# Kernel tuning notes

Hardware: AMD Instinct MI355X
Metric: run time of the kernel (lower is better)

Reference implementation:

```python
import jax, jax.numpy as jnp
import numpy as np

B, S, H, A = 64, 200, 256, 16
CAPS_LAYERS = 3
NEG = -1e9
LN_EPS = 1e-12


def _layernorm(x, g, b):
    mu = jnp.mean(x, axis=-1, keepdims=True)
    var = jnp.mean(jnp.square(x - mu), axis=-1, keepdims=True)
    return (x - mu) / jnp.sqrt(var + LN_EPS) * g + b


def setup_inputs() -> dict:
    key = jax.random.key(0)
    ks = jax.random.split(key, 10)
    s = 0.02  # initializer_range
    return {
        "item_emb": jax.random.normal(ks[0], (B, S, H), jnp.float32),
        "item_seq": jax.random.randint(ks[1], (B, S), 0, 50000),
        "time_seq": jax.random.randint(ks[2], (B, S, 2), 0, 14),
        "W_lin": s * jax.random.normal(ks[3], (H, H), jnp.float32),
        "b_lin": jnp.zeros((H,), jnp.float32),
        "aspect_embs": s * jax.random.normal(ks[4], (A, H), jnp.float32),
        "pos_emb": s * jax.random.normal(ks[5], (S, H), jnp.float32),
        "tdt_emb": s * jax.random.normal(ks[6], (14, H), jnp.float32),
        "tdn_emb": s * jax.random.normal(ks[7], (14, H), jnp.float32),
        "Wa1": s * jax.random.normal(ks[8], (H, H), jnp.float32),
        "ba1": jnp.zeros((H,), jnp.float32),
        "Wa2": s * jax.random.normal(ks[9], (H,), jnp.float32),
        "ba2": jnp.zeros((1,), jnp.float32),
        "ln_g": jnp.ones((H,), jnp.float32),
        "ln_b": jnp.zeros((H,), jnp.float32),
    }


def reference(item_emb, item_seq, time_seq, W_lin, b_lin, aspect_embs,
              pos_emb, tdt_emb, tdn_emb, Wa1, ba1, Wa2, ba2, ln_g, ln_b):
    b, s = item_emb.shape[0], item_emb.shape[1]
    pad = item_seq == 0  # [B,S]

    # ---- TimeAwareAttention (seq_output has a singleton neighbor dim in torch) ----
    td = tdt_emb[time_seq[:, :, 0]] + tdn_emb[time_seq[:, :, 1]]       # [B,S,H]
    tma_in = pos_emb[None, :s] + item_emb + td                          # [B,S,H]
    h = tma_in @ Wa1 + ba1
    h = jnp.where(h >= 0, h, 0.01 * h)                                  # LeakyReLU
    w = h @ Wa2 + ba2[0]                                                # [B,S]
    w = jnp.where(pad, NEG, w)
    tma = jax.nn.softmax(w, axis=-1)                                    # [B,S]

    # ---- gating (eval: clean gates) ----
    gates = jnp.einsum('bsh,ah->bsa', item_emb, aspect_embs)            # [B,S,A]
    idx = jnp.argmax(gates, axis=-1)                                    # topk k=1, [B,S]

    src = jnp.where(pad, 0.0, 1.0)
    counts = jnp.zeros((b, A), jnp.float32).at[jnp.arange(b)[:, None], idx].add(src)
    aspect_mask = counts == 0                                           # [B,A]

    # ---- item transform (dropout = identity in eval) ----
    moe = _layernorm(jnp.tanh(item_emb @ W_lin + b_lin) + item_emb, ln_g, ln_b)  # [B,S,H]

    # ---- capsule routing ----
    bij = gates
    cap = jnp.broadcast_to(aspect_embs[None], (b, A, H))
    for _ in range(CAPS_LAYERS):
        cij = jnp.where(aspect_mask[:, None, :], NEG, bij)
        cij = jax.nn.softmax(cij, axis=-1)
        cij = jnp.where(pad[:, :, None], 0.0, cij)                      # [B,S,A]
        cap = jnp.einsum('bsa,bsh,bs->bah', cij, moe, tma)              # [B,A,H]
        n2 = jnp.sum(jnp.square(cap), axis=-1, keepdims=True)
        cap = n2 / (1.0 + n2) / jnp.sqrt(n2 + 1e-9) * cap               # squash
        bij = bij + jnp.einsum('bsh,bah->bsa', moe, cap)

    # ---- gather activated interests / activation positions ----
    activated = cap[jnp.arange(b)[:, None], idx]                        # [B,S,H]
    seq_pos = jnp.where(pad, 0, jnp.arange(1, s + 1)[None, :]).astype(jnp.float32)
    act_mat = jnp.full((b, s, A), -1.0, jnp.float32)
    act_mat = act_mat.at[jnp.arange(b)[:, None], jnp.arange(s)[None, :], idx].set(seq_pos)
    act_mat = jnp.where(pad[:, :, None], -1.0, act_mat)
    max_pos = jnp.max(act_mat, axis=1)                                  # [B,A]
    aspects_item_idx = jnp.where(max_pos > -1.0, max_pos - 1.0, max_pos)

    gates_sm = jax.nn.softmax(gates, axis=-1)
    return (cap, gates_sm, aspect_mask, activated, aspects_item_idx, idx[:, :, None])
```

## Files before the change

### kernel.cpp

```cpp
#include <hip/hip_runtime.h>

#define B_ 64
#define S_ 200
#define H_ 256
#define A_ 16
#define M_ (B_*S_)
#define NEGV (-1000000000.0f)

typedef unsigned short ushortT;
typedef __attribute__((ext_vector_type(8))) short short8;
typedef __attribute__((ext_vector_type(4))) float f32x4;

__device__ __forceinline__ ushortT bf16u(float f) {
  unsigned int u = __builtin_bit_cast(unsigned int, f);
  unsigned int r = (u + 0x7fffu + ((u >> 16) & 1u)) >> 16;
  return (ushortT)r;
}
__device__ __forceinline__ float bf2f(ushortT u) {
  unsigned int v = ((unsigned int)u) << 16;
  return __builtin_bit_cast(float, v);
}

__global__ __launch_bounds__(256) void prepT_kernel(
    const float* __restrict__ Wa1, const float* __restrict__ W_lin,
    ushortT* __restrict__ Wa1T, ushortT* __restrict__ WlinT)
{
  __shared__ float T[64*65];
  const int blk = blockIdx.x, t = threadIdx.x;
  int wsel = blk >> 4;
  int tile = blk & 15;
  const float* W = wsel ? W_lin : Wa1;
  ushortT* WT = wsel ? WlinT : Wa1T;
  int tr = (tile >> 2) * 64, tc = (tile & 3) * 64;
  #pragma unroll
  for (int p = 0; p < 16; ++p) {
    int r = p*4 + (t >> 6);
    int c = t & 63;
    T[c*65 + r] = W[(tr + r)*H_ + tc + c];
  }
  __syncthreads();
  #pragma unroll
  for (int p = 0; p < 16; ++p) {
    int n = p*4 + (t >> 6);
    int k = t & 63;
    WT[(tc + n)*H_ + tr + k] = bf16u(T[n*65 + k]);
  }
}

__global__ __launch_bounds__(512) void fused_kernel(
    const float* __restrict__ item, const int* __restrict__ iseq,
    const int* __restrict__ tseq, const float* __restrict__ pos,
    const float* __restrict__ tdt, const float* __restrict__ tdn,
    const float* __restrict__ asp,
    const ushortT* __restrict__ Wa1T, const ushortT* __restrict__ WlinT,
    const float* __restrict__ ba1, const float* __restrict__ Wa2,
    const float* __restrict__ ba2, const float* __restrict__ b_lin,
    const float* __restrict__ g_ln, const float* __restrict__ b_ln,
    float* __restrict__ w_out, ushortT* __restrict__ moe_outB,
    float* __restrict__ graw, float* __restrict__ gates_sm,
    float* __restrict__ idxf)
{
  __shared__ __align__(16) ushortT smem[51200];
  __shared__ int sL[64], ttL[64], tnL[64];
  __shared__ float wp[2][64], ln1[2][64], ln2[2][64], mus[64], rss[64];

  const int t = threadIdx.x;
  const int m0 = blockIdx.x * 64;
  const int lane = t & 63, w = t >> 6;
  const int g = w >> 2, wl = w & 3;
  const int wm = wl >> 1, wn = wl & 1;
  const int col = lane & 15;
  const int rg  = lane >> 4;

  if (t < 64) {
    int m = m0 + t;
    sL[t]  = m % S_;
    ttL[t] = tseq[2*m];
    tnL[t] = tseq[2*m+1];
  }
  __syncthreads();

  const int arow = t >> 3;
  const int ac4  = (t & 7) * 4;
  const int nr   = t >> 1;
  const int kh   = (t & 1) * 16;
  const int srow = sL[arow], trow = ttL[arow], nrow = tnL[arow];

  ushortT* const Atma0 = smem;
  ushortT* const Aitm0 = smem + 5120;
  ushortT* const B0b   = smem + 10240;
  ushortT* const B1b   = smem + 30720;

  float4 pi = *(const float4*)&item[(size_t)(m0+arow)*H_ + ac4];
  float4 pp = *(const float4*)&pos[srow*H_ + ac4];
  float4 pt = *(const float4*)&tdt[trow*H_ + ac4];
  float4 pn = *(const float4*)&tdn[nrow*H_ + ac4];
  uint4 b0a = *(const uint4*)&Wa1T[(size_t)nr*H_ + kh];
  uint4 b0b = *(const uint4*)&Wa1T[(size_t)nr*H_ + kh + 8];
  uint4 b1a = *(const uint4*)&WlinT[(size_t)nr*H_ + kh];
  uint4 b1b = *(const uint4*)&WlinT[(size_t)nr*H_ + kh + 8];
  {
    union { ushortT u[4]; uint2 v; } ci, ct;
    ci.u[0] = bf16u(pi.x); ci.u[1] = bf16u(pi.y);
    ci.u[2] = bf16u(pi.z); ci.u[3] = bf16u(pi.w);
    ct.u[0] = bf16u(pi.x + pp.x + pt.x + pn.x);
    ct.u[1] = bf16u(pi.y + pp.y + pt.y + pn.y);
    ct.u[2] = bf16u(pi.z + pp.z + pt.z + pn.z);
    ct.u[3] = bf16u(pi.w + pp.w + pt.w + pn.w);
    *(uint2*)&Aitm0[arow*40 + ac4] = ci.v;
    *(uint2*)&Atma0[arow*40 + ac4] = ct.v;
    *(uint4*)&B0b[nr*40 + kh]     = b0a;
    *(uint4*)&B0b[nr*40 + kh + 8] = b0b;
    *(uint4*)&B1b[nr*40 + kh]     = b1a;
    *(uint4*)&B1b[nr*40 + kh + 8] = b1b;
  }
  __syncthreads();

  f32x4 acc[2][8];
  #pragma unroll
  for (int r = 0; r < 2; ++r)
    #pragma unroll
    for (int q = 0; q < 8; ++q) acc[r][q] = (f32x4){0.f,0.f,0.f,0.f};

  #pragma unroll
  for (int ks = 0; ks < 8; ++ks) {
    if (ks < 7) {
      const int k1 = (ks + 1) * 32;
      pi = *(const float4*)&item[(size_t)(m0+arow)*H_ + k1 + ac4];
      pp = *(const float4*)&pos[srow*H_ + k1 + ac4];
      pt = *(const float4*)&tdt[trow*H_ + k1 + ac4];
      pn = *(const float4*)&tdn[nrow*H_ + k1 + ac4];
      b0a = *(const uint4*)&Wa1T[(size_t)nr*H_ + k1 + kh];
      b0b = *(const uint4*)&Wa1T[(size_t)nr*H_ + k1 + kh + 8];
      b1a = *(const uint4*)&WlinT[(size_t)nr*H_ + k1 + kh];
      b1b = *(const uint4*)&WlinT[(size_t)nr*H_ + k1 + kh + 8];
    }
    {
      const int p = ks & 1;
      const ushortT* Ab = (g ? Aitm0 : Atma0) + p*2560;
      const ushortT* Bb = (g ? B1b : B0b) + p*10240;
      short8 af0 = *(const short8*)&Ab[(wm*32 + col)*40 + rg*8];
      short8 af1 = *(const short8*)&Ab[(wm*32 + 16 + col)*40 + rg*8];
      #pragma unroll
      for (int q = 0; q < 8; ++q) {
        short8 bf = *(const short8*)&Bb[(wn*128 + q*16 + col)*40 + rg*8];
        acc[0][q] = __builtin_amdgcn_mfma_f32_16x16x32_bf16(af0, bf, acc[0][q], 0, 0, 0);
        acc[1][q] = __builtin_amdgcn_mfma_f32_16x16x32_bf16(af1, bf, acc[1][q], 0, 0, 0);
      }
    }
    if (ks < 7) {
      const int p = (ks + 1) & 1;
      union { ushortT u[4]; uint2 v; } ci, ct;
      ci.u[0] = bf16u(pi.x); ci.u[1] = bf16u(pi.y);
      ci.u[2] = bf16u(pi.z); ci.u[3] = bf16u(pi.w);
      ct.u[0] = bf16u(pi.x + pp.x + pt.x + pn.x);
      ct.u[1] = bf16u(pi.y + pp.y + pt.y + pn.y);
      ct.u[2] = bf16u(pi.z + pp.z + pt.z + pn.z);
      ct.u[3] = bf16u(pi.w + pp.w + pt.w + pn.w);
      *(uint2*)&(Aitm0 + p*2560)[arow*40 + ac4] = ci.v;
      *(uint2*)&(Atma0 + p*2560)[arow*40 + ac4] = ct.v;
      ushortT* B0w = B0b + p*10240;
      ushortT* B1w = B1b + p*10240;
      *(uint4*)&B0w[nr*40 + kh]     = b0a;
      *(uint4*)&B0w[nr*40 + kh + 8] = b0b;
      *(uint4*)&B1w[nr*40 + kh]     = b1a;
      *(uint4*)&B1w[nr*40 + kh + 8] = b1b;
    }
    __syncthreads();
  }

  float* aspl = (float*)smem;
  float* gL   = (float*)smem + 4160;
  #pragma unroll
  for (int i = 0; i < 2; ++i) {
    int e = t + 512*i;
    int r = e >> 6, c = e & 63;
    *(float4*)&aspl[r*260 + 4*c] = *(const float4*)&asp[r*H_ + 4*c];
  }

  float glv[8], bbv[8];
  if (g == 0) {
    float bav[8], wav[8];
    #pragma unroll
    for (int q = 0; q < 8; ++q) {
      int n = wn*128 + q*16 + col;
      bav[q] = ba1[n]; wav[q] = Wa2[n];
    }
    #pragma unroll
    for (int r = 0; r < 2; ++r)
      #pragma unroll
      for (int j = 0; j < 4; ++j) {
        float p = 0.f;
        #pragma unroll
        for (int q = 0; q < 8; ++q) {
          float h = acc[r][q][j] + bav[q];
          h = (h >= 0.f) ? h : 0.01f*h;
          p += h * wav[q];
        }
        #pragma unroll
        for (int mk = 1; mk < 16; mk <<= 1) p += __shfl_xor(p, mk);
        if (col == 0) wp[wn][wm*32 + r*16 + rg*4 + j] = p;
      }
  } else {
    float blv[8];
    #pragma unroll
    for (int q = 0; q < 8; ++q) {
      int n = wn*128 + q*16 + col;
      blv[q] = b_lin[n]; glv[q] = g_ln[n]; bbv[q] = b_ln[n];
    }
    #pragma unroll
    for (int r = 0; r < 2; ++r)
      #pragma unroll
      for (int j = 0; j < 4; ++j) {
        int row = wm*32 + r*16 + rg*4 + j;
        float s1 = 0.f, s2 = 0.f;
        #pragma unroll
        for (int q = 0; q < 8; ++q) {
          int n = wn*128 + q*16 + col;
          float vv = tanhf(acc[r][q][j] + blv[q]) + item[(size_t)(m0+row)*H_ + n];
          acc[r][q][j] = vv; s1 += vv; s2 += vv*vv;
        }
        #pragma unroll
        for (int mk = 1; mk < 16; mk <<= 1) {
          s1 += __shfl_xor(s1, mk);
          s2 += __shfl_xor(s2, mk);
        }
        if (col == 0) { ln1[wn][row] = s1; ln2[wn][row] = s2; }
      }
  }
  __syncthreads();
  if (t < 64) {
    int row = t, m = m0 + row;
    w_out[m] = (iseq[m] == 0) ? NEGV : (wp[0][row] + wp[1][row] + ba2[0]);
  } else if (t < 128) {
    int row = t - 64;
    float s1 = ln1[0][row] + ln1[1][row];
    float s2 = ln2[0][row] + ln2[1][row];
    float mu  = s1 * (1.0f/H_);
    float var = s2 * (1.0f/H_) - mu*mu;
    mus[row] = mu;
    rss[row] = 1.0f / sqrtf(fmaxf(var, 0.f) + 1e-12f);
  }
  __syncthreads();
  if (g == 1) {
    #pragma unroll
    for (int r = 0; r < 2; ++r)
      #pragma unroll
      for (int j = 0; j < 4; ++j) {
        int row = wm*32 + r*16 + rg*4 + j;
        int m = m0 + row;
        float mu = mus[row], rs = rss[row];
        #pragma unroll
        for (int q = 0; q < 8; ++q) {
          int n = wn*128 + q*16 + col;
          moe_outB[(size_t)m*H_ + n] = bf16u((acc[r][q][j] - mu)*rs*glv[q] + bbv[q]);
        }
      }
  }

  {
    const int a  = t & 15;
    const int r2 = (t >> 4) * 2;
    float ga = 0.f, gb = 0.f;
    const float* x0p = &item[(size_t)(m0 + r2)*H_];
    const float* x1p = &item[(size_t)(m0 + r2 + 1)*H_];
    #pragma unroll 8
    for (int k4 = 0; k4 < 64; ++k4) {
      float4 av = *(const float4*)&aspl[a*260 + 4*k4];
      float4 x0 = *(const float4*)&x0p[4*k4];
      float4 x1 = *(const float4*)&x1p[4*k4];
      ga += x0.x*av.x + x0.y*av.y + x0.z*av.z + x0.w*av.w;
      gb += x1.x*av.x + x1.y*av.y + x1.z*av.z + x1.w*av.w;
    }
    gL[r2*20 + a]       = ga;
    gL[(r2 + 1)*20 + a] = gb;
  }
  __syncthreads();
  if (t < 64) {
    float row[16];
    #pragma unroll
    for (int a = 0; a < 16; ++a) row[a] = gL[t*20 + a];
    float best = row[0]; int bi = 0;
    #pragma unroll
    for (int a = 1; a < 16; ++a)
      if (row[a] > best) { best = row[a]; bi = a; }
    idxf[m0 + t] = (float)bi;
    float mx = row[0];
    #pragma unroll
    for (int a = 1; a < 16; ++a) mx = fmaxf(mx, row[a]);
    float ex[16], sm = 0.f;
    #pragma unroll
    for (int a = 0; a < 16; ++a) { ex[a] = expf(row[a] - mx); sm += ex[a]; }
    float inv = 1.f / sm;
    #pragma unroll
    for (int q = 0; q < 4; ++q) {
      float4 rv; rv.x = row[4*q]; rv.y = row[4*q+1]; rv.z = row[4*q+2]; rv.w = row[4*q+3];
      *(float4*)&graw[(m0+t)*A_ + 4*q] = rv;
      float4 o; o.x = ex[4*q]*inv; o.y = ex[4*q+1]*inv; o.z = ex[4*q+2]*inv; o.w = ex[4*q+3]*inv;
      *(float4*)&gates_sm[(m0+t)*A_ + 4*q] = o;
    }
  }
}

__device__ __forceinline__ float blk_max(float v, float* red) {
  #pragma unroll
  for (int mk = 32; mk; mk >>= 1) v = fmaxf(v, __shfl_xor(v, mk));
  int t = threadIdx.x;
  if ((t & 63) == 0) red[t >> 6] = v;
  __syncthreads();
  if (t < 64) {
    float x = (t < 16) ? red[t] : -3.0e38f;
    #pragma unroll
    for (int mk = 8; mk; mk >>= 1) x = fmaxf(x, __shfl_xor(x, mk));
    if (t == 0) red[0] = x;
  }
  __syncthreads();
  float r = red[0];
  __syncthreads();
  return r;
}

__device__ __forceinline__ float blk_sum(float v, float* red) {
  #pragma unroll
  for (int mk = 32; mk; mk >>= 1) v += __shfl_xor(v, mk);
  int t = threadIdx.x;
  if ((t & 63) == 0) red[t >> 6] = v;
  __syncthreads();
  if (t < 64) {
    float x = (t < 16) ? red[t] : 0.f;
    #pragma unroll
    for (int mk = 8; mk; mk >>= 1) x += __shfl_xor(x, mk);
    if (t == 0) red[0] = x;
  }
  __syncthreads();
  float r = red[0];
  __syncthreads();
  return r;
}

#define WGSTR 232
#define CBSTR 260
#define CLSTR 252

__global__ __launch_bounds__(1024) void phaseC_kernel(
    const int* __restrict__ iseq, const float* __restrict__ w_in,
    const ushortT* __restrict__ moeB, const float* __restrict__ idxf,
    const float* __restrict__ graw,
    float* __restrict__ cap_out,
    float* __restrict__ mask_out,
    float* __restrict__ aidx_out)
{
  __shared__ ushortT moeTr[57344];
  __shared__ ushortT wgtT[16*WGSTR];
  __shared__ ushortT capB[16*CBSTR];
  __shared__ float bij[4032];
  __shared__ float n2p[16*17];
  __shared__ float n2s[16];
  __shared__ float tmaL[S_];
  __shared__ float red[16];
  __shared__ float maskf[A_];
  __shared__ int counts[A_], maxpos[A_];
  __shared__ int idxl[S_];
  __shared__ int padl[S_];

  const int t = threadIdx.x;
  const int b = blockIdx.x;
  const int base = b * S_;
  const int lane = t & 63, w = t >> 6;
  const int la = lane & 15, lg = lane >> 4;

  #pragma unroll
  for (int u = 0; u < 4; ++u) {
    int e = t + 1024*u;
    if (e < 3584) {
      int ht = e & 15, s = e >> 4;
      int ks = s >> 5, s4l = (s >> 2) & 7, sr = s & 3;
      int bp = (s4l & 1) ? 4 + (s4l >> 1) : (s4l >> 1);
      int li = ((ht*7 + ks)*8 + bp)*64 + sr*16;
      if (s < S_) {
        const ushortT* gp = &moeB[((size_t)(base + s))*H_ + ht*16];
        *(uint4*)&moeTr[li]     = *(const uint4*)gp;
        *(uint4*)&moeTr[li + 8] = *(const uint4*)(gp + 8);
      } else {
        uint4 z = {0,0,0,0};
        *(uint4*)&moeTr[li] = z; *(uint4*)&moeTr[li + 8] = z;
      }
    }
  }
  if (t < 512) {
    int a = t >> 5, s = 200 + (t & 31);
    wgtT[a*WGSTR + s] = 0;
  }

  if (t < A_) { counts[t] = 0; maxpos[t] = -1; }
  float wv = -3.0e38f;
  if (t < S_) {
    int s = t;
    padl[s] = (iseq[base+s] == 0) ? 1 : 0;
    idxl[s] = (int)idxf[base+s];
    wv = w_in[base+s];
    #pragma unroll
    for (int q = 0; q < 4; ++q)
      *(float4*)&bij[s*20 + 4*q] = *(const float4*)&graw[(base+s)*A_ + 4*q];
  }
  __syncthreads();

  short8 a2[7];
  {
    unsigned vA = (unsigned)(w*7168 + lane*8);
    #pragma unroll
    for (int ks = 0; ks < 7; ++ks) {
      long long r0, r1;
      asm volatile(
        "ds_read_b64_tr_b16 %0, %2\n\t"
        "ds_read_b64_tr_b16 %1, %2 offset:512\n\t"
        "s_waitcnt lgkmcnt(0)"
        : "=&v"(r0), "=&v"(r1) : "v"(vA + (unsigned)(ks*1024)) : "memory");
      __builtin_amdgcn_sched_barrier(0);
      union { short8 v; long long q[2]; } uu;
      uu.q[0] = r0; uu.q[1] = r1;
      a2[ks] = uu.v;
    }
  }

  if (t < S_ && !padl[t]) {
    atomicAdd(&counts[idxl[t]], 1);
    atomicMax(&maxpos[idxl[t]], t + 1);
  }
  float mxw = blk_max(wv, red);
  float ev = (t < S_) ? expf(wv - mxw) : 0.f;
  float sw = blk_sum(ev, red);
  if (t < S_) tmaL[t] = ev / sw;
  __syncthreads();
  if (t < A_) {
    int c = counts[t];
    float mkv = (c == 0) ? 1.f : 0.f;
    maskf[t] = mkv;
    mask_out[b*A_ + t] = mkv;
    int mp = maxpos[t];
    aidx_out[b*A_ + t] = (mp > 0) ? (float)(mp - 1) : -1.f;
  }
  __syncthreads();

  for (int iter = 0; iter < 3; ++iter) {
    #pragma unroll
    for (int pass = 0; pass < 4; ++pass) {
      int s = pass*64 + (t >> 4);
      int a = t & 15;
      if (s < S_) {
        float v = bij[s*20 + a];
        v = (maskf[a] > 0.5f) ? NEGV : v;
        float mx = v;
        #pragma unroll
        for (int mk = 1; mk < 16; mk <<= 1) mx = fmaxf(mx, __shfl_xor(mx, mk));
        float e = expf(v - mx);
        float sm = e;
        #pragma unroll
        for (int mk = 1; mk < 16; mk <<= 1) sm += __shfl_xor(sm, mk);
        float sc = (padl[s] ? 0.f : tmaL[s]) / sm;
        wgtT[a*WGSTR + s] = bf16u(e*sc);
      }
    }
    __syncthreads();

    f32x4 acc = (f32x4){0.f,0.f,0.f,0.f};
    #pragma unroll
    for (int ks = 0; ks < 7; ++ks) {
      short8 bf = *(const short8*)&wgtT[la*WGSTR + ks*32 + lg*8];
      acc = __builtin_amdgcn_mfma_f32_16x16x32_bf16(a2[ks], bf, acc, 0, 0, 0);
    }
    {
      float n2 = acc[0]*acc[0] + acc[1]*acc[1] + acc[2]*acc[2] + acc[3]*acc[3];
      n2 += __shfl_xor(n2, 16);
      n2 += __shfl_xor(n2, 32);
      if (lane < 16) n2p[w*17 + lane] = n2;
    }
    __syncthreads();
    if (t < 16) {
      float sv = 0.f;
      #pragma unroll
      for (int w2 = 0; w2 < 16; ++w2) sv += n2p[w2*17 + t];
      n2s[t] = sv / (1.f + sv) / sqrtf(sv + 1e-9f);
    }
    __syncthreads();
    {
      float sc = n2s[la];
      if (iter < 2) {
        #pragma unroll
        for (int r = 0; r < 4; ++r)
          capB[la*CBSTR + w*16 + lg*4 + r] = bf16u(acc[r]*sc);
      } else {
        float* capl = bij;
        #pragma unroll
        for (int r = 0; r < 4; ++r)
          capl[la*CLSTR + w*16 + lg*4 + r] = acc[r]*sc;
      }
    }
    __syncthreads();

    if (iter < 2) {
      if (w < 13) {
        int sR = w*16 + la;
        int ksS = sR >> 5, s4l = (sR >> 2) & 7, sr = sR & 3;
        int bp = (s4l & 1) ? 4 + (s4l >> 1) : (s4l >> 1);
        int laneA = ksS*512 + bp*64 + sr*16 + (lg & 1)*8 + (lg >> 1)*3584;
        f32x4 accS = (f32x4){0.f,0.f,0.f,0.f};
        #pragma unroll
        for (int k4 = 0; k4 < 8; ++k4) {
          short8 am = *(const short8*)&moeTr[laneA + k4*7168];
          short8 bc = *(const short8*)&capB[la*CBSTR + k4*32 + lg*8];
          accS = __builtin_amdgcn_mfma_f32_16x16x32_bf16(am, bc, accS, 0, 0, 0);
        }
        int sW = w*16 + lg*4;
        #pragma unroll
        for (int r = 0; r < 4; ++r)
          if (sW + r < S_) bij[(sW + r)*20 + la] += accS[r];
      }
      __syncthreads();
    }
  }

  {
    const float* capl = bij;
    int a = t >> 6, h4 = t & 63;
    float4 v = *(const float4*)&capl[a*CLSTR + 4*h4];
    *(float4*)&cap_out[((size_t)b*A_ + a)*H_ + 4*h4] = v;
  }
}

__global__ __launch_bounds__(256) void gather_kernel(
    const float* __restrict__ capv, const float* __restrict__ idxf,
    float* __restrict__ act)
{
  int e4 = blockIdx.x * 256 + threadIdx.x;
  int m = e4 >> 6, h4 = e4 & 63;
  int b = m / S_;
  int id = (int)idxf[m];
  float4 v = *(const float4*)&capv[((b*A_) + id)*H_ + 4*h4];
  *(float4*)&act[(size_t)4*e4] = v;
}

extern "C" void kernel_launch(void* const* d_in, const int* in_sizes, int n_in,
                              void* d_out, int out_size, void* d_ws, size_t ws_size,
                              hipStream_t stream) {
  (void)in_sizes; (void)n_in; (void)out_size; (void)ws_size;
  const float* item  = (const float*)d_in[0];
  const int*   iseq  = (const int*)d_in[1];
  const int*   tseq  = (const int*)d_in[2];
  const float* W_lin = (const float*)d_in[3];
  const float* b_lin = (const float*)d_in[4];
  const float* asp   = (const float*)d_in[5];
  const float* pos   = (const float*)d_in[6];
  const float* tdt   = (const float*)d_in[7];
  const float* tdn   = (const float*)d_in[8];
  const float* Wa1   = (const float*)d_in[9];
  const float* ba1   = (const float*)d_in[10];
  const float* Wa2   = (const float*)d_in[11];
  const float* ba2   = (const float*)d_in[12];
  const float* g_ln  = (const float*)d_in[13];
  const float* b_ln  = (const float*)d_in[14];

  float* out    = (float*)d_out;
  float* cap_o  = out;
  float* gate_o = out + 262144;
  float* mask_o = out + 466944;
  float* act_o  = out + 467968;
  float* aidx_o = out + 3744768;
  float* idx_o  = out + 3745792;

  ushortT* moeB  = (ushortT*)d_ws;
  ushortT* Wa1T  = (ushortT*)((char*)d_ws + 6553600);
  ushortT* WlinT = (ushortT*)((char*)d_ws + 6553600 + 131072);
  float*   w_ws  = (float*)((char*)d_ws + 6553600 + 262144);
  float*   graw  = (float*)((char*)d_ws + 6553600 + 262144 + 51200);

  prepT_kernel<<<32, 256, 0, stream>>>(Wa1, W_lin, Wa1T, WlinT);
  fused_kernel<<<200, 512, 0, stream>>>(item, iseq, tseq, pos, tdt, tdn, asp,
      Wa1T, WlinT, ba1, Wa2, ba2, b_lin, g_ln, b_ln, w_ws, moeB,
      graw, gate_o, idx_o);
  phaseC_kernel<<<B_, 1024, 0, stream>>>(iseq, w_ws, moeB, idx_o, graw,
      cap_o, mask_o, aidx_o);
  gather_kernel<<<(M_*H_/4)/256, 256, 0, stream>>>(cap_o, idx_o, act_o);
}
```

Measured before the change: 62.73 us.

## Load GEMM B fragments directly to registers and fuse gather into phaseC

The fused kernel now loads the transposed weight fragments for its MFMAs straight from global memory into double-buffered registers instead of staging them through shared memory. This cuts LDS usage from about 100KB to about 22KB and adds a launch bound requesting two blocks per CU. Separately, the activated-interest gather is folded into the end of phaseC, which reads capsules from shared memory and drops a separate kernel launch. The trade-offs are more global weight traffic per wave (each wave re-reads its fragments) and more register pressure, plus a longer tail in phaseC with only 64 blocks writing the large act output.

New measurement: 66.71 us. 6.3% more time.

```diff
diff --git a/kernel.cpp b/kernel.cpp
--- a/kernel.cpp
+++ b/kernel.cpp
@@ -47,7 +47,7 @@
   }
 }
 
-__global__ __launch_bounds__(512) void fused_kernel(
+__global__ __launch_bounds__(512, 2) void fused_kernel(
     const float* __restrict__ item, const int* __restrict__ iseq,
     const int* __restrict__ tseq, const float* __restrict__ pos,
     const float* __restrict__ tdt, const float* __restrict__ tdn,
@@ -60,7 +60,7 @@
     float* __restrict__ graw, float* __restrict__ gates_sm,
     float* __restrict__ idxf)
 {
-  __shared__ __align__(16) ushortT smem[51200];
+  __shared__ __align__(16) ushortT smem[11264];
   __shared__ int sL[64], ttL[64], tnL[64];
   __shared__ float wp[2][64], ln1[2][64], ln2[2][64], mus[64], rss[64];
 
@@ -82,23 +82,22 @@
 
   const int arow = t >> 3;
   const int ac4  = (t & 7) * 4;
-  const int nr   = t >> 1;
-  const int kh   = (t & 1) * 16;
   const int srow = sL[arow], trow = ttL[arow], nrow = tnL[arow];
 
   ushortT* const Atma0 = smem;
   ushortT* const Aitm0 = smem + 5120;
-  ushortT* const B0b   = smem + 10240;
-  ushortT* const B1b   = smem + 30720;
+
+  const ushortT* __restrict__ WTp = g ? WlinT : Wa1T;
 
   float4 pi = *(const float4*)&item[(size_t)(m0+arow)*H_ + ac4];
   float4 pp = *(const float4*)&pos[srow*H_ + ac4];
   float4 pt = *(const float4*)&tdt[trow*H_ + ac4];
   float4 pn = *(const float4*)&tdn[nrow*H_ + ac4];
-  uint4 b0a = *(const uint4*)&Wa1T[(size_t)nr*H_ + kh];
-  uint4 b0b = *(const uint4*)&Wa1T[(size_t)nr*H_ + kh + 8];
-  uint4 b1a = *(const uint4*)&WlinT[(size_t)nr*H_ + kh];
-  uint4 b1b = *(const uint4*)&WlinT[(size_t)nr*H_ + kh + 8];
+  short8 bfr[2][8];
+  #pragma unroll
+  for (int q = 0; q < 8; ++q)
+    bfr[0][q] = *(const short8*)&WTp[(size_t)(wn*128 + q*16 + col)*H_ + rg*8];
+
   {
     union { ushortT u[4]; uint2 v; } ci, ct;
     ci.u[0] = bf16u(pi.x); ci.u[1] = bf16u(pi.y);
@@ -109,10 +108,6 @@
     ct.u[3] = bf16u(pi.w + pp.w + pt.w + pn.w);
     *(uint2*)&Aitm0[arow*40 + ac4] = ci.v;
     *(uint2*)&Atma0[arow*40 + ac4] = ct.v;
-    *(uint4*)&B0b[nr*40 + kh]     = b0a;
-    *(uint4*)&B0b[nr*40 + kh + 8] = b0b;
-    *(uint4*)&B1b[nr*40 + kh]     = b1a;
-    *(uint4*)&B1b[nr*40 + kh + 8] = b1b;
   }
   __syncthreads();
 
@@ -130,22 +125,19 @@
       pp = *(const float4*)&pos[srow*H_ + k1 + ac4];
       pt = *(const float4*)&tdt[trow*H_ + k1 + ac4];
       pn = *(const float4*)&tdn[nrow*H_ + k1 + ac4];
-      b0a = *(const uint4*)&Wa1T[(size_t)nr*H_ + k1 + kh];
-      b0b = *(const uint4*)&Wa1T[(size_t)nr*H_ + k1 + kh + 8];
-      b1a = *(const uint4*)&WlinT[(size_t)nr*H_ + k1 + kh];
-      b1b = *(const uint4*)&WlinT[(size_t)nr*H_ + k1 + kh + 8];
+      #pragma unroll
+      for (int q = 0; q < 8; ++q)
+        bfr[(ks+1)&1][q] = *(const short8*)&WTp[(size_t)(wn*128 + q*16 + col)*H_ + k1 + rg*8];
     }
     {
       const int p = ks & 1;
       const ushortT* Ab = (g ? Aitm0 : Atma0) + p*2560;
-      const ushortT* Bb = (g ? B1b : B0b) + p*10240;
       short8 af0 = *(const short8*)&Ab[(wm*32 + col)*40 + rg*8];
       short8 af1 = *(const short8*)&Ab[(wm*32 + 16 + col)*40 + rg*8];
       #pragma unroll
       for (int q = 0; q < 8; ++q) {
-        short8 bf = *(const short8*)&Bb[(wn*128 + q*16 + col)*40 + rg*8];
-        acc[0][q] = __builtin_amdgcn_mfma_f32_16x16x32_bf16(af0, bf, acc[0][q], 0, 0, 0);
-        acc[1][q] = __builtin_amdgcn_mfma_f32_16x16x32_bf16(af1, bf, acc[1][q], 0, 0, 0);
+        acc[0][q] = __builtin_amdgcn_mfma_f32_16x16x32_bf16(af0, bfr[ks&1][q], acc[0][q], 0, 0, 0);
+        acc[1][q] = __builtin_amdgcn_mfma_f32_16x16x32_bf16(af1, bfr[ks&1][q], acc[1][q], 0, 0, 0);
       }
     }
     if (ks < 7) {
@@ -159,12 +151,6 @@
       ct.u[3] = bf16u(pi.w + pp.w + pt.w + pn.w);
       *(uint2*)&(Aitm0 + p*2560)[arow*40 + ac4] = ci.v;
       *(uint2*)&(Atma0 + p*2560)[arow*40 + ac4] = ct.v;
-      ushortT* B0w = B0b + p*10240;
-      ushortT* B1w = B1b + p*10240;
-      *(uint4*)&B0w[nr*40 + kh]     = b0a;
-      *(uint4*)&B0w[nr*40 + kh + 8] = b0b;
-      *(uint4*)&B1w[nr*40 + kh]     = b1a;
-      *(uint4*)&B1w[nr*40 + kh + 8] = b1b;
     }
     __syncthreads();
   }
@@ -348,7 +334,8 @@
     const float* __restrict__ graw,
     float* __restrict__ cap_out,
     float* __restrict__ mask_out,
-    float* __restrict__ aidx_out)
+    float* __restrict__ aidx_out,
+    float* __restrict__ act_out)
 {
   __shared__ ushortT moeTr[57344];
   __shared__ ushortT wgtT[16*WGSTR];
@@ -525,19 +512,11 @@
     int a = t >> 6, h4 = t & 63;
     float4 v = *(const float4*)&capl[a*CLSTR + 4*h4];
     *(float4*)&cap_out[((size_t)b*A_ + a)*H_ + 4*h4] = v;
-  }
-}
-
-__global__ __launch_bounds__(256) void gather_kernel(
-    const float* __restrict__ capv, const float* __restrict__ idxf,
-    float* __restrict__ act)
-{
-  int e4 = blockIdx.x * 256 + threadIdx.x;
-  int m = e4 >> 6, h4 = e4 & 63;
-  int b = m / S_;
-  int id = (int)idxf[m];
-  float4 v = *(const float4*)&capv[((b*A_) + id)*H_ + 4*h4];
-  *(float4*)&act[(size_t)4*e4] = v;
+    for (int s = t >> 6; s < S_; s += 16) {
+      float4 av = *(const float4*)&capl[idxl[s]*CLSTR + 4*h4];
+      *(float4*)&act_out[((size_t)base + s)*H_ + 4*h4] = av;
+    }
+  }
 }
 
 extern "C" void kernel_launch(void* const* d_in, const int* in_sizes, int n_in,
@@ -579,6 +558,5 @@
       Wa1T, WlinT, ba1, Wa2, ba2, b_lin, g_ln, b_ln, w_ws, moeB,
       graw, gate_o, idx_o);
   phaseC_kernel<<<B_, 1024, 0, stream>>>(iseq, w_ws, moeB, idx_o, graw,
-      cap_o, mask_o, aidx_o);
-  gather_kernel<<<(M_*H_/4)/256, 256, 0, stream>>>(cap_o, idx_o, act_o);
-}
+      cap_o, mask_o, aidx_o, act_o);
+}
```
